# Kernel optimization log

Hardware: AMD Instinct MI355X
Metric: run time of the kernel (lower is better)

Reference implementation:

```python
import jax, jax.numpy as jnp
import numpy as np

N_NODES = 50000
N_EDGES = 1_600_000
N_REL = 8
D_IN = 128
D_OUT = 128


def _unique_edges(rng, n_nodes, n_rel, n_edges):
    # Torch module clamps the dense adjacency to 0/1, so duplicate
    # (rel, src, dst) triples collapse; generate unique edges so the
    # edge-list formulation matches exactly.
    m = 2 * n_edges
    src = rng.integers(0, n_nodes, m)
    dst = rng.integers(0, n_nodes, m)
    et = rng.integers(0, n_rel, m)
    key = (et.astype(np.int64) * n_nodes + src) * n_nodes + dst
    _, idx = np.unique(key, return_index=True)
    idx = np.sort(idx)[:n_edges]
    return src[idx], dst[idx], et[idx]


def setup_inputs() -> dict:
    key = jax.random.key(0)
    kx, kw, kr, kb = jax.random.split(key, 4)
    rng = np.random.default_rng(0)
    src, dst, et = _unique_edges(rng, N_NODES, N_REL, N_EDGES)
    bound = 1.0 / np.sqrt(D_OUT)
    return {
        "x": jax.random.normal(kx, (N_NODES, D_IN), dtype=jnp.float32),
        "edge_index": jnp.asarray(np.stack([src, dst]), dtype=jnp.int64),
        "edge_type": jnp.asarray(et, dtype=jnp.int64),
        "weight": jax.random.uniform(kw, (N_REL, D_OUT, D_IN), minval=-bound, maxval=bound, dtype=jnp.float32),
        "root": jax.random.uniform(kr, (D_OUT, D_IN), minval=-bound, maxval=bound, dtype=jnp.float32),
        "bias": jax.random.uniform(kb, (D_OUT,), minval=-bound, maxval=bound, dtype=jnp.float32),
    }


def reference(x, edge_index, edge_type, weight, root, bias):
    # Math identical to: adj[l, src, dst] = 1; adj row-normalized (mean);
    # out = sum_r norm_adj_r @ x @ W_r^T + x @ root^T + bias.
    n_rel, d_out, d_in = weight.shape
    n_nodes = x.shape[0]
    src = edge_index[0]
    dst = edge_index[1]
    seg = (edge_type * n_nodes + src).astype(jnp.int32)  # segment per (rel, node)
    num_seg = n_rel * n_nodes
    # sum of neighbor features per (relation, node): [R*N, d_in]
    agg = jax.ops.segment_sum(x[dst], seg, num_segments=num_seg)
    deg = jax.ops.segment_sum(jnp.ones((src.shape[0],), dtype=x.dtype), seg, num_segments=num_seg)
    norm = jnp.where(deg > 0, 1.0 / deg, 0.0)[:, None]  # mean aggr, nan_to_num(0)
    agg = (agg * norm).reshape(n_rel, n_nodes, d_in)
    out = jnp.einsum('rnd,rod->no', agg, weight)
    out = out + x @ root.T + bias[None]
    return out
```

## Files before the change

kernel.cpp:

```cpp
#include <hip/hip_runtime.h>


#define D 128
#define SCAN_CHUNK 2048
#define SEG_BITS 9
#define SEGS_PER_BUCKET 512
#define NBLK 256
#define NDEG 32

typedef __attribute__((ext_vector_type(8))) short short8;
typedef __attribute__((ext_vector_type(4))) float v4f;
typedef __attribute__((ext_vector_type(2))) float f32x2;
typedef __attribute__((ext_vector_type(4))) unsigned uint4v;

#define GLOAD_LDS16(gptr, lptr) \
    __builtin_amdgcn_global_load_lds((const __attribute__((address_space(1))) void*)(gptr), \
                                     (__attribute__((address_space(3))) void*)(lptr), 16, 0, 0)

__device__ __forceinline__ unsigned short f2b(float f) {
    union { float f; unsigned u; } v; v.f = f;
    unsigned r = v.u + 0x7fffu + ((v.u >> 16) & 1u);
    return (unsigned short)(r >> 16);
}
__device__ __forceinline__ float blo(unsigned u) {
    union { unsigned u; float f; } v; v.u = u << 16; return v.f;
}
__device__ __forceinline__ float bhi(unsigned u) {
    union { unsigned u; float f; } v; v.u = u & 0xffff0000u; return v.f;
}

__global__ void cvt_bf16_all(const float* __restrict__ x, long long nx,
                             const float* __restrict__ w, long long nw,
                             const float* __restrict__ root, long long nr,
                             unsigned short* __restrict__ Abuf,
                             unsigned short* __restrict__ wB, size_t SLs) {
    long long i = ((long long)blockIdx.x * blockDim.x + threadIdx.x) * 4;
    if (i < nx) {
        float4 v = *(const float4*)(x + i);
        uint2 p;
        p.x = (unsigned)f2b(v.x) | ((unsigned)f2b(v.y) << 16);
        p.y = (unsigned)f2b(v.z) | ((unsigned)f2b(v.w) << 16);
        long long n = i >> 7;
        int d = (int)(i & 127);
        size_t o = (size_t)((d >> 5) * 9 + 8) * SLs + (size_t)n * 32 + (d & 31);
        *(uint2*)(Abuf + o) = p;
        return;
    }
    const float* src;
    unsigned short* dst;
    long long j;
    if (i < nx + nw) { src = w; dst = wB; j = i - nx; }
    else if (i < nx + nw + nr) { src = root; dst = wB + nw; j = i - nx - nw; }
    else return;
    float4 v = *(const float4*)(src + j);
    uint2 p;
    p.x = (unsigned)f2b(v.x) | ((unsigned)f2b(v.y) << 16);
    p.y = (unsigned)f2b(v.z) | ((unsigned)f2b(v.w) << 16);
    *(uint2*)(dst + j) = p;
}

__global__ __launch_bounds__(256)
void histA(const int* __restrict__ ei, const int* __restrict__ et,
           int* __restrict__ blockHist, int nE, int nN, int B, int epb) {
    __shared__ int lh[1024];
    const int tid = threadIdx.x;
    for (int b = tid; b < B; b += 256) lh[b] = 0;
    __syncthreads();
    const int base = blockIdx.x * epb;
    const int lim = min(base + epb, nE);
    for (int e = base + tid * 4; e < lim; e += 1024) {
        if (e + 4 <= lim) {
            int4 s = *(const int4*)(ei + e);
            int4 t = *(const int4*)(et + e);
            atomicAdd(&lh[(t.x * nN + s.x) >> SEG_BITS], 1);
            atomicAdd(&lh[(t.y * nN + s.y) >> SEG_BITS], 1);
            atomicAdd(&lh[(t.z * nN + s.z) >> SEG_BITS], 1);
            atomicAdd(&lh[(t.w * nN + s.w) >> SEG_BITS], 1);
        } else {
            for (int k = e; k < lim; k++)
                atomicAdd(&lh[(et[k] * nN + ei[k]) >> SEG_BITS], 1);
        }
    }
    __syncthreads();
    for (int b = tid; b < B; b += 256)
        blockHist[b * NBLK + blockIdx.x] = lh[b];
}

__global__ __launch_bounds__(256)
void scan1(const int* __restrict__ in, int* __restrict__ excl,
           int* __restrict__ blockSums, int n) {
    __shared__ int t[256];
    const int tid = threadIdx.x;
    const int base = blockIdx.x * SCAN_CHUNK + tid * 8;
    int v[8];
    int tot = 0;
#pragma unroll
    for (int i = 0; i < 8; i++) {
        v[i] = (base + i < n) ? in[base + i] : 0;
        tot += v[i];
    }
    t[tid] = tot;
    __syncthreads();
    for (int off = 1; off < 256; off <<= 1) {
        int add = (tid >= off) ? t[tid - off] : 0;
        __syncthreads();
        t[tid] += add;
        __syncthreads();
    }
    int run = t[tid] - tot;
#pragma unroll
    for (int i = 0; i < 8; i++) {
        if (base + i < n) excl[base + i] = run;
        run += v[i];
    }
    if (tid == 255) blockSums[blockIdx.x] = t[255];
}

__global__ __launch_bounds__(256)
void scan2(int* __restrict__ blockSums, int nb) {
    __shared__ int t[256];
    const int tid = threadIdx.x;
    int v = (tid < nb) ? blockSums[tid] : 0;
    t[tid] = v;
    __syncthreads();
    for (int off = 1; off < 256; off <<= 1) {
        int add = (tid >= off) ? t[tid - off] : 0;
        __syncthreads();
        t[tid] += add;
        __syncthreads();
    }
    if (tid < nb) blockSums[tid] = t[tid] - v;
}

__global__ __launch_bounds__(256)
void scatterA(const int* __restrict__ ei, const int* __restrict__ et,
              const int* __restrict__ scanned, const int* __restrict__ blockSums,
              unsigned* __restrict__ bucketEdges,
              int nE, int nN, int B, int epb) {
    __shared__ int cur[1024];
    const int tid = threadIdx.x;
    for (int b = tid; b < B; b += 256) {
        int idx = b * NBLK + blockIdx.x;
        cur[b] = scanned[idx] + blockSums[idx >> 11];
    }
    __syncthreads();
    const int base = blockIdx.x * epb;
    const int lim = min(base + epb, nE);
    for (int e = base + tid * 4; e < lim; e += 1024) {
        if (e + 4 <= lim) {
            int4 s = *(const int4*)(ei + e);
            int4 t = *(const int4*)(et + e);
            int4 d = *(const int4*)(ei + nE + e);
            int sg;
            sg = t.x * nN + s.x;
            bucketEdges[atomicAdd(&cur[sg >> SEG_BITS], 1)] =
                ((unsigned)(sg & (SEGS_PER_BUCKET - 1)) << 16) | (unsigned)d.x;
            sg = t.y * nN + s.y;
            bucketEdges[atomicAdd(&cur[sg >> SEG_BITS], 1)] =
                ((unsigned)(sg & (SEGS_PER_BUCKET - 1)) << 16) | (unsigned)d.y;
            sg = t.z * nN + s.z;
            bucketEdges[atomicAdd(&cur[sg >> SEG_BITS], 1)] =
                ((unsigned)(sg & (SEGS_PER_BUCKET - 1)) << 16) | (unsigned)d.z;
            sg = t.w * nN + s.w;
            bucketEdges[atomicAdd(&cur[sg >> SEG_BITS], 1)] =
                ((unsigned)(sg & (SEGS_PER_BUCKET - 1)) << 16) | (unsigned)d.w;
        } else {
            for (int k = e; k < lim; k++) {
                int sg = et[k] * nN + ei[k];
                bucketEdges[atomicAdd(&cur[sg >> SEG_BITS], 1)] =
                    ((unsigned)(sg & (SEGS_PER_BUCKET - 1)) << 16) | (unsigned)ei[nE + k];
            }
        }
    }
}

__global__ __launch_bounds__(256)
void segOff(const unsigned* __restrict__ bucketEdges, const int* __restrict__ scanned,
            const int* __restrict__ blockSums,
            int4* __restrict__ permRec, unsigned short* __restrict__ sortedDst,
            int* __restrict__ permMax, int nE, int numSeg, int B) {
    __shared__ int lh[SEGS_PER_BUCKET];
    __shared__ int sc[256];
    __shared__ int lcur[SEGS_PER_BUCKET];
    __shared__ int dcnt[256];
    __shared__ int dbase[256];
    __shared__ int smax[32];
    const int tid = threadIdx.x;
    const int b = blockIdx.x;
    const int i0 = b * NBLK;
    const int eBase = scanned[i0] + blockSums[i0 >> 11];
    int eEnd = nE;
    if (b + 1 < B) {
        const int i1 = (b + 1) * NBLK;
        eEnd = scanned[i1] + blockSums[i1 >> 11];
    }
    const int segBase = b * SEGS_PER_BUCKET;
    const int segLim = min(SEGS_PER_BUCKET, numSeg - segBase);

    lh[2 * tid] = 0; lh[2 * tid + 1] = 0;
    dcnt[tid] = 0;
    if (tid < 32) smax[tid] = 0;
    __syncthreads();
    for (int i = eBase + tid; i < eEnd; i += 256)
        atomicAdd(&lh[bucketEdges[i] >> 16], 1);
    __syncthreads();
    const int li0 = 2 * tid, li1 = 2 * tid + 1;
    const int sub = li0 >> 6;
    int a0 = lh[li0], a1 = lh[li1];
    int b0 = min(a0, NDEG - 1), b1 = min(a1, NDEG - 1), r0 = 0, r1 = 0;
    if (li0 < segLim) r0 = atomicAdd(&dcnt[sub * NDEG + b0], 1);
    if (li1 < segLim) r1 = atomicAdd(&dcnt[sub * NDEG + b1], 1);
    sc[tid] = a0 + a1;
    __syncthreads();
    for (int o = 1; o < 256; o <<= 1) {
        int add = (tid >= o) ? sc[tid - o] : 0;
        __syncthreads();
        sc[tid] += add;
        __syncthreads();
    }
    int pairBase = sc[tid] - (a0 + a1);
    int g0 = eBase + pairBase;
    int g1 = g0 + a0;
    lcur[li0] = g0;
    lcur[li1] = g1;
    if (tid < 8) {
        int run = 0;
#pragma unroll
        for (int k = 0; k < NDEG; k++) { dbase[tid * NDEG + k] = run; run += dcnt[tid * NDEG + k]; }
    }
    __syncthreads();
    if (li0 < segLim) {
        int rk = dbase[sub * NDEG + b0] + r0;
        permRec[segBase + sub * 64 + rk] = make_int4(g0, a0, segBase + li0, 0);
        atomicMax(&smax[(sub << 2) + (rk >> 4)], a0);
    }
    if (li1 < segLim) {
        int rk = dbase[sub * NDEG + b1] + r1;
        permRec[segBase + sub * 64 + rk] = make_int4(g1, a1, segBase + li1, 0);
        atomicMax(&smax[(sub << 2) + (rk >> 4)], a1);
    }
    for (int i = eBase + tid; i < eEnd; i += 256) {
        unsigned u = bucketEdges[i];
        int pos = atomicAdd(&lcur[u >> 16], 1);
        sortedDst[pos] = (unsigned short)(u & 0xFFFFu);
    }
    __syncthreads();
    if (tid < 32) permMax[b * 32 + tid] = smax[tid];
}

__global__ __launch_bounds__(256)
void rgcn_gather(const unsigned short* __restrict__ Abase,
                 const unsigned short* __restrict__ sortedDst,
                 const int4* __restrict__ permRec,
                 const int* __restrict__ permMax,
                 unsigned short* __restrict__ Abuf, int nN, int numSeg,
                 size_t SLs, unsigned long long M) {
    const int tid = threadIdx.x;
    const int lane = tid & 63;
    const int idx4 = lane & 3;
    const int grp = lane >> 2;
    const int wv = tid >> 6;
    const int gsi0 = blockIdx.x * 128 + wv * 32 + grp;
    const int gsi1 = gsi0 + 16;
    const int sl = blockIdx.y;
    const bool v0 = (gsi0 < numSeg);
    const bool v1 = (gsi1 < numSeg);

    int4 rc0 = v0 ? permRec[gsi0] : make_int4(0, 0, 0, 0);
    int4 rc1 = v1 ? permRec[gsi1] : make_int4(0, 0, 0, 0);
    int mx0 = v0 ? permMax[gsi0 >> 4] : 0;
    int mx1 = v1 ? permMax[gsi1 >> 4] : 0;
    mx0 = __builtin_amdgcn_readfirstlane(mx0);
    mx1 = __builtin_amdgcn_readfirstlane(mx1);

    const int start0 = rc0.x, cnt0 = v0 ? rc0.y : 0, seg0 = rc0.z;
    const int start1 = rc1.x, cnt1 = v1 ? rc1.y : 0, seg1 = rc1.z;

    f32x2 a0[4], a1[4];
#pragma unroll
    for (int i = 0; i < 4; i++) { a0[i] = (f32x2){0.f, 0.f}; a1[i] = (f32x2){0.f, 0.f}; }

    const unsigned short* xSlab = Abase + (size_t)(sl * 9 + 8) * SLs + idx4 * 8;

    const int mxm = max(mx0, mx1);
    for (int b = 0; b < mxm; b += 4) {
        uint4v w0[4], w1[4];
        int myD0 = 0, myD1 = 0;
        if (b < mx0) myD0 = (b + idx4 < cnt0) ? (int)sortedDst[start0 + b + idx4] : 0;
        if (b < mx1) myD1 = (b + idx4 < cnt1) ? (int)sortedDst[start1 + b + idx4] : 0;
        if (b < mx0) {
#pragma unroll
            for (int j = 0; j < 4; j++) {
                int dst = __shfl(myD0, grp * 4 + j);
                bool act = (b + j < cnt0);
                w0[j] = act ? *(const uint4v*)(xSlab + ((size_t)dst << 5))
                            : (uint4v){0u, 0u, 0u, 0u};
            }
        }
        if (b < mx1) {
#pragma unroll
            for (int j = 0; j < 4; j++) {
                int dst = __shfl(myD1, grp * 4 + j);
                bool act = (b + j < cnt1);
                w1[j] = act ? *(const uint4v*)(xSlab + ((size_t)dst << 5))
                            : (uint4v){0u, 0u, 0u, 0u};
            }
        }
        if (b < mx0) {
#pragma unroll
            for (int j = 0; j < 4; j++) {
                f32x2 t0 = (f32x2){blo(w0[j].x), bhi(w0[j].x)};
                f32x2 t1 = (f32x2){blo(w0[j].y), bhi(w0[j].y)};
                f32x2 t2 = (f32x2){blo(w0[j].z), bhi(w0[j].z)};
                f32x2 t3 = (f32x2){blo(w0[j].w), bhi(w0[j].w)};
                asm("v_pk_add_f32 %0, %0, %1" : "+v"(a0[0]) : "v"(t0));
                asm("v_pk_add_f32 %0, %0, %1" : "+v"(a0[1]) : "v"(t1));
                asm("v_pk_add_f32 %0, %0, %1" : "+v"(a0[2]) : "v"(t2));
                asm("v_pk_add_f32 %0, %0, %1" : "+v"(a0[3]) : "v"(t3));
            }
        }
        if (b < mx1) {
#pragma unroll
            for (int j = 0; j < 4; j++) {
                f32x2 t0 = (f32x2){blo(w1[j].x), bhi(w1[j].x)};
                f32x2 t1 = (f32x2){blo(w1[j].y), bhi(w1[j].y)};
                f32x2 t2 = (f32x2){blo(w1[j].z), bhi(w1[j].z)};
                f32x2 t3 = (f32x2){blo(w1[j].w), bhi(w1[j].w)};
                asm("v_pk_add_f32 %0, %0, %1" : "+v"(a1[0]) : "v"(t0));
                asm("v_pk_add_f32 %0, %0, %1" : "+v"(a1[1]) : "v"(t1));
                asm("v_pk_add_f32 %0, %0, %1" : "+v"(a1[2]) : "v"(t2));
                asm("v_pk_add_f32 %0, %0, %1" : "+v"(a1[3]) : "v"(t3));
            }
        }
    }

    if (v0) {
        float s = cnt0 > 0 ? 1.0f / (float)cnt0 : 0.f;
        const int r = (int)(((unsigned long long)seg0 * M) >> 48);
        const int n = seg0 - r * nN;
        unsigned p0, p1, p2, p3;
        float e0, e1;
        e0 = a0[0].x * s; e1 = a0[0].y * s;
        asm("v_cvt_pk_bf16_f32 %0, %1, %2" : "=v"(p0) : "v"(e0), "v"(e1));
        e0 = a0[1].x * s; e1 = a0[1].y * s;
        asm("v_cvt_pk_bf16_f32 %0, %1, %2" : "=v"(p1) : "v"(e0), "v"(e1));
        e0 = a0[2].x * s; e1 = a0[2].y * s;
        asm("v_cvt_pk_bf16_f32 %0, %1, %2" : "=v"(p2) : "v"(e0), "v"(e1));
        e0 = a0[3].x * s; e1 = a0[3].y * s;
        asm("v_cvt_pk_bf16_f32 %0, %1, %2" : "=v"(p3) : "v"(e0), "v"(e1));
        uint4v pkt = (uint4v){p0, p1, p2, p3};
        __builtin_nontemporal_store(pkt,
            (uint4v*)(Abuf + (size_t)(sl * 9 + r) * SLs + (size_t)n * 32 + idx4 * 8));
    }
    if (v1) {
        float s = cnt1 > 0 ? 1.0f / (float)cnt1 : 0.f;
        const int r = (int)(((unsigned long long)seg1 * M) >> 48);
        const int n = seg1 - r * nN;
        unsigned p0, p1, p2, p3;
        float e0, e1;
        e0 = a1[0].x * s; e1 = a1[0].y * s;
        asm("v_cvt_pk_bf16_f32 %0, %1, %2" : "=v"(p0) : "v"(e0), "v"(e1));
        e0 = a1[1].x * s; e1 = a1[1].y * s;
        asm("v_cvt_pk_bf16_f32 %0, %1, %2" : "=v"(p1) : "v"(e0), "v"(e1));
        e0 = a1[2].x * s; e1 = a1[2].y * s;
        asm("v_cvt_pk_bf16_f32 %0, %1, %2" : "=v"(p2) : "v"(e0), "v"(e1));
        e0 = a1[3].x * s; e1 = a1[3].y * s;
        asm("v_cvt_pk_bf16_f32 %0, %1, %2" : "=v"(p3) : "v"(e0), "v"(e1));
        uint4v pkt = (uint4v){p0, p1, p2, p3};
        __builtin_nontemporal_store(pkt,
            (uint4v*)(Abuf + (size_t)(sl * 9 + r) * SLs + (size_t)n * 32 + idx4 * 8));
    }
}

__global__ __launch_bounds__(256)
void rgcn_gemm_mfma(const unsigned short* __restrict__ A,
                    const unsigned short* __restrict__ wB,
                    const float* __restrict__ bias,
                    float* __restrict__ out, int nN, int nRel, size_t SLs) {
    __shared__ __align__(16) unsigned short As[2][128 * 64];
    __shared__ __align__(16) unsigned short Bs[2][128 * 64];
    const int tid = threadIdx.x;
    const int wave = tid >> 6;
    const int lane = tid & 63;
    const int wm = wave & 1;
    const int wn = wave >> 1;
    const int m16 = lane & 15;
    const int q = lane >> 4;
    const int row0 = blockIdx.x * 128;

    v4f acc[4][4];
#pragma unroll
    for (int i = 0; i < 4; i++)
#pragma unroll
        for (int j = 0; j < 4; j++) acc[i][j] = (v4f){0.f, 0.f, 0.f, 0.f};

    const int sw = m16 & 7;
    int aoff[4][2], boff[4][2];
#pragma unroll
    for (int mt = 0; mt < 4; mt++) {
        int row = wm * 64 + mt * 16 + m16;
#pragma unroll
        for (int kb = 0; kb < 2; kb++)
            aoff[mt][kb] = row * 64 + (((kb * 4 + q) ^ sw) * 8);
    }
#pragma unroll
    for (int nt = 0; nt < 4; nt++) {
        int o = wn * 64 + nt * 16 + m16;
#pragma unroll
        for (int kb = 0; kb < 2; kb++)
            boff[nt][kb] = o * 64 + (((kb * 4 + q) ^ sw) * 8);
    }

    const int l8 = lane >> 3;
    const int gd = (lane & 7) ^ l8;
    size_t aB[4];
#pragma unroll
    for (int i = 0; i < 4; i++)
        aB[i] = (size_t)((gd >> 2) * 9) * SLs
              + (size_t)(row0 + wave * 32 + i * 8 + l8) * 32 + (gd & 3) * 8;
    const size_t bBase = (size_t)(wave * 32 + l8) * D + gd * 8;

    const int nT = 2 * (nRel + 1);

#define STAGE(buf, t) do { \
        const int s_ = (t) >> 1, h_ = (t) & 1; \
        const size_t hs_ = (size_t)h_ * 18 * SLs + (size_t)s_ * SLs; \
        const unsigned short* gb_ = wB + (size_t)s_ * (D * D) + h_ * 64 + bBase; \
        GLOAD_LDS16(A + aB[0] + hs_, &As[buf][(wave * 4 + 0) * 512]); \
        GLOAD_LDS16(A + aB[1] + hs_, &As[buf][(wave * 4 + 1) * 512]); \
        GLOAD_LDS16(A + aB[2] + hs_, &As[buf][(wave * 4 + 2) * 512]); \
        GLOAD_LDS16(A + aB[3] + hs_, &As[buf][(wave * 4 + 3) * 512]); \
        GLOAD_LDS16(gb_,        &Bs[buf][(wave * 4 + 0) * 512]); \
        GLOAD_LDS16(gb_ + 1024, &Bs[buf][(wave * 4 + 1) * 512]); \
        GLOAD_LDS16(gb_ + 2048, &Bs[buf][(wave * 4 + 2) * 512]); \
        GLOAD_LDS16(gb_ + 3072, &Bs[buf][(wave * 4 + 3) * 512]); \
    } while (0)

    STAGE(0, 0);
    __syncthreads();
    int cur = 0;
    for (int t = 0; t < nT; ++t) {
        if (t + 1 < nT) STAGE(cur ^ 1, t + 1);
        const unsigned short* Ab = As[cur];
        const unsigned short* Bb = Bs[cur];
#pragma unroll
        for (int kb = 0; kb < 2; kb++) {
            short8 a[4], b[4];
#pragma unroll
            for (int mt = 0; mt < 4; mt++)
                a[mt] = *(const short8*)&Ab[aoff[mt][kb]];
#pragma unroll
            for (int nt = 0; nt < 4; nt++)
                b[nt] = *(const short8*)&Bb[boff[nt][kb]];
#pragma unroll
            for (int mt = 0; mt < 4; mt++)
#pragma unroll
                for (int nt = 0; nt < 4; nt++)
                    acc[mt][nt] = __builtin_amdgcn_mfma_f32_16x16x32_bf16(
                        a[mt], b[nt], acc[mt][nt], 0, 0, 0);
        }
        __syncthreads();
        cur ^= 1;
    }
#undef STAGE

#pragma unroll
    for (int mt = 0; mt < 4; mt++) {
#pragma unroll
        for (int nt = 0; nt < 4; nt++) {
            int col = wn * 64 + nt * 16 + m16;
            float bi = bias[col];
#pragma unroll
            for (int reg = 0; reg < 4; reg++) {
                int rrow = row0 + wm * 64 + mt * 16 + q * 4 + reg;
                if (rrow < nN)
                    out[(size_t)rrow * D + col] = acc[mt][nt][reg] + bi;
            }
        }
    }
}

extern "C" void kernel_launch(void* const* d_in, const int* in_sizes, int n_in,
                              void* d_out, int out_size, void* d_ws, size_t ws_size,
                              hipStream_t stream) {
    const float* x    = (const float*)d_in[0];
    const int*   ei   = (const int*)d_in[1];
    const int*   et   = (const int*)d_in[2];
    const float* w    = (const float*)d_in[3];
    const float* root = (const float*)d_in[4];
    const float* bias = (const float*)d_in[5];
    float* out = (float*)d_out;

    const int nN   = in_sizes[0] / D;
    const int nE   = in_sizes[2];
    const int nRel = in_sizes[3] / (D * D);
    const int numSeg = nRel * nN;
    const int B = (numSeg + SEGS_PER_BUCKET - 1) >> SEG_BITS;
    const int nBH = B * NBLK;
    const int epb = (((nE + NBLK - 1) / NBLK) + 3) & ~3;
    const int nNalloc = (nN + 127) & ~127;
    const size_t SLs = (size_t)nNalloc * 32;
    const unsigned long long M = ((1ULL << 48) + nN - 1) / nN;

    char* p = (char*)d_ws;
    unsigned* bucketEdges   = (unsigned*)p;        p += (size_t)nE * sizeof(unsigned);
    unsigned short* sortedDst = (unsigned short*)p; p += (size_t)nE * sizeof(unsigned short);
    p = (char*)(((uintptr_t)p + 255) & ~(uintptr_t)255);
    int* blockHist = (int*)p;  p += (size_t)nBH * sizeof(int);
    int* scanned   = (int*)p;  p += (size_t)nBH * sizeof(int);
    int* blockSums = (int*)p;  p += 256 * sizeof(int);
    p = (char*)(((uintptr_t)p + 255) & ~(uintptr_t)255);
    int4* permRec  = (int4*)p; p += (size_t)numSeg * sizeof(int4);
    int* permMax   = (int*)p;  p += (size_t)B * 32 * sizeof(int);
    p = (char*)(((uintptr_t)p + 255) & ~(uintptr_t)255);
    unsigned short* wBc  = (unsigned short*)p;  p += (size_t)(nRel + 1) * D * D * sizeof(unsigned short);
    p = (char*)(((uintptr_t)p + 255) & ~(uintptr_t)255);
    unsigned short* Abuf = (unsigned short*)p;

    const int nScanBlocks = (nBH + SCAN_CHUNK - 1) / SCAN_CHUNK;

    histA<<<NBLK, 256, 0, stream>>>(ei, et, blockHist, nE, nN, B, epb);
    scan1<<<nScanBlocks, 256, 0, stream>>>(blockHist, scanned, blockSums, nBH);
    scan2<<<1, 256, 0, stream>>>(blockSums, nScanBlocks);
    scatterA<<<NBLK, 256, 0, stream>>>(ei, et, scanned, blockSums, bucketEdges, nE, nN, B, epb);
    segOff<<<B, 256, 0, stream>>>(bucketEdges, scanned, blockSums, permRec, sortedDst, permMax,
                                  nE, numSeg, B);

    long long nx = (long long)nN * D;
    long long nw = (long long)nRel * D * D;
    long long nr = (long long)D * D;
    long long ncvt = (nx + nw + nr) / 4;
    cvt_bf16_all<<<(int)((ncvt + 255) / 256), 256, 0, stream>>>(x, nx, w, nw, root, nr,
                                                                Abuf, wBc, SLs);

    dim3 gg((numSeg + 127) / 128, 4);
    rgcn_gather<<<gg, 256, 0, stream>>>(Abuf, sortedDst, permRec, permMax, Abuf, nN, numSeg,
                                        SLs, M);

    rgcn_gemm_mfma<<<(nN + 127) / 128, 256, 0, stream>>>(Abuf, wBc, bias, out, nN, nRel, SLs);
}
```

Measured before the change: 225.7 us.

## Fuse bf16 conversion into histogram launch and fold block-sum scan into consumers

The bf16 conversion of x and the weights now runs as extra blocks of the histogram kernel, so both share one launch and overlap. The one-block scan2 kernel is removed; scatterA and segOff each redo the small block-sum prefix scan in shared memory. The gather's nontemporal stores become regular stores, so Abuf may stay in cache for the GEMM. This cuts two launches and their serialization, at the cost of redundant scan work in every block and a 128-entry limit on scan blocks.

```diff
diff --git a/kernel.cpp b/kernel.cpp
--- a/kernel.cpp
+++ b/kernel.cpp
@@ -29,41 +29,42 @@
     union { unsigned u; float f; } v; v.u = u & 0xffff0000u; return v.f;
 }
 
-__global__ void cvt_bf16_all(const float* __restrict__ x, long long nx,
-                             const float* __restrict__ w, long long nw,
-                             const float* __restrict__ root, long long nr,
-                             unsigned short* __restrict__ Abuf,
-                             unsigned short* __restrict__ wB, size_t SLs) {
-    long long i = ((long long)blockIdx.x * blockDim.x + threadIdx.x) * 4;
-    if (i < nx) {
-        float4 v = *(const float4*)(x + i);
+__global__ __launch_bounds__(256)
+void histA_cvt(const int* __restrict__ ei, const int* __restrict__ et,
+               int* __restrict__ blockHist, int nE, int nN, int B, int epb,
+               const float* __restrict__ x, long long nx,
+               const float* __restrict__ w, long long nw,
+               const float* __restrict__ root, long long nr,
+               unsigned short* __restrict__ Abuf,
+               unsigned short* __restrict__ wB, size_t SLs) {
+    __shared__ int lh[1024];
+    const int tid = threadIdx.x;
+    if (blockIdx.x >= NBLK) {
+        long long i = ((long long)(blockIdx.x - NBLK) * blockDim.x + tid) * 4;
+        if (i < nx) {
+            float4 v = *(const float4*)(x + i);
+            uint2 p;
+            p.x = (unsigned)f2b(v.x) | ((unsigned)f2b(v.y) << 16);
+            p.y = (unsigned)f2b(v.z) | ((unsigned)f2b(v.w) << 16);
+            long long n = i >> 7;
+            int d = (int)(i & 127);
+            size_t o = (size_t)((d >> 5) * 9 + 8) * SLs + (size_t)n * 32 + (d & 31);
+            *(uint2*)(Abuf + o) = p;
+            return;
+        }
+        const float* src;
+        unsigned short* dst;
+        long long j;
+        if (i < nx + nw) { src = w; dst = wB; j = i - nx; }
+        else if (i < nx + nw + nr) { src = root; dst = wB + nw; j = i - nx - nw; }
+        else return;
+        float4 v = *(const float4*)(src + j);
         uint2 p;
         p.x = (unsigned)f2b(v.x) | ((unsigned)f2b(v.y) << 16);
         p.y = (unsigned)f2b(v.z) | ((unsigned)f2b(v.w) << 16);
-        long long n = i >> 7;
-        int d = (int)(i & 127);
-        size_t o = (size_t)((d >> 5) * 9 + 8) * SLs + (size_t)n * 32 + (d & 31);
-        *(uint2*)(Abuf + o) = p;
+        *(uint2*)(dst + j) = p;
         return;
     }
-    const float* src;
-    unsigned short* dst;
-    long long j;
-    if (i < nx + nw) { src = w; dst = wB; j = i - nx; }
-    else if (i < nx + nw + nr) { src = root; dst = wB + nw; j = i - nx - nw; }
-    else return;
-    float4 v = *(const float4*)(src + j);
-    uint2 p;
-    p.x = (unsigned)f2b(v.x) | ((unsigned)f2b(v.y) << 16);
-    p.y = (unsigned)f2b(v.z) | ((unsigned)f2b(v.w) << 16);
-    *(uint2*)(dst + j) = p;
-}
-
-__global__ __launch_bounds__(256)
-void histA(const int* __restrict__ ei, const int* __restrict__ et,
-           int* __restrict__ blockHist, int nE, int nN, int B, int epb) {
-    __shared__ int lh[1024];
-    const int tid = threadIdx.x;
     for (int b = tid; b < B; b += 256) lh[b] = 0;
     __syncthreads();
     const int base = blockIdx.x * epb;
@@ -117,31 +118,27 @@
 }
 
 __global__ __launch_bounds__(256)
-void scan2(int* __restrict__ blockSums, int nb) {
-    __shared__ int t[256];
-    const int tid = threadIdx.x;
-    int v = (tid < nb) ? blockSums[tid] : 0;
-    t[tid] = v;
-    __syncthreads();
-    for (int off = 1; off < 256; off <<= 1) {
-        int add = (tid >= off) ? t[tid - off] : 0;
-        __syncthreads();
-        t[tid] += add;
-        __syncthreads();
-    }
-    if (tid < nb) blockSums[tid] = t[tid] - v;
-}
-
-__global__ __launch_bounds__(256)
 void scatterA(const int* __restrict__ ei, const int* __restrict__ et,
               const int* __restrict__ scanned, const int* __restrict__ blockSums,
               unsigned* __restrict__ bucketEdges,
-              int nE, int nN, int B, int epb) {
+              int nE, int nN, int B, int epb, int nSB) {
     __shared__ int cur[1024];
+    __shared__ int bs[128];
     const int tid = threadIdx.x;
+    int myv = 0;
+    if (tid < 128) { myv = (tid < nSB) ? blockSums[tid] : 0; bs[tid] = myv; }
+    __syncthreads();
+    for (int o = 1; o < 128; o <<= 1) {
+        int add = (tid >= o && tid < 128) ? bs[tid - o] : 0;
+        __syncthreads();
+        if (tid < 128) bs[tid] += add;
+        __syncthreads();
+    }
+    if (tid < 128) bs[tid] -= myv;
+    __syncthreads();
     for (int b = tid; b < B; b += 256) {
         int idx = b * NBLK + blockIdx.x;
-        cur[b] = scanned[idx] + blockSums[idx >> 11];
+        cur[b] = scanned[idx] + bs[idx >> 11];
     }
     __syncthreads();
     const int base = blockIdx.x * epb;
@@ -178,29 +175,40 @@
 void segOff(const unsigned* __restrict__ bucketEdges, const int* __restrict__ scanned,
             const int* __restrict__ blockSums,
             int4* __restrict__ permRec, unsigned short* __restrict__ sortedDst,
-            int* __restrict__ permMax, int nE, int numSeg, int B) {
+            int* __restrict__ permMax, int nE, int numSeg, int B, int nSB) {
     __shared__ int lh[SEGS_PER_BUCKET];
     __shared__ int sc[256];
     __shared__ int lcur[SEGS_PER_BUCKET];
     __shared__ int dcnt[256];
     __shared__ int dbase[256];
     __shared__ int smax[32];
+    __shared__ int bs[128];
     const int tid = threadIdx.x;
     const int b = blockIdx.x;
+    int myv = 0;
+    if (tid < 128) { myv = (tid < nSB) ? blockSums[tid] : 0; bs[tid] = myv; }
+    lh[2 * tid] = 0; lh[2 * tid + 1] = 0;
+    dcnt[tid] = 0;
+    if (tid < 32) smax[tid] = 0;
+    __syncthreads();
+    for (int o = 1; o < 128; o <<= 1) {
+        int add = (tid >= o && tid < 128) ? bs[tid - o] : 0;
+        __syncthreads();
+        if (tid < 128) bs[tid] += add;
+        __syncthreads();
+    }
+    if (tid < 128) bs[tid] -= myv;
+    __syncthreads();
     const int i0 = b * NBLK;
-    const int eBase = scanned[i0] + blockSums[i0 >> 11];
+    const int eBase = scanned[i0] + bs[i0 >> 11];
     int eEnd = nE;
     if (b + 1 < B) {
         const int i1 = (b + 1) * NBLK;
-        eEnd = scanned[i1] + blockSums[i1 >> 11];
+        eEnd = scanned[i1] + bs[i1 >> 11];
     }
     const int segBase = b * SEGS_PER_BUCKET;
     const int segLim = min(SEGS_PER_BUCKET, numSeg - segBase);
 
-    lh[2 * tid] = 0; lh[2 * tid + 1] = 0;
-    dcnt[tid] = 0;
-    if (tid < 32) smax[tid] = 0;
-    __syncthreads();
     for (int i = eBase + tid; i < eEnd; i += 256)
         atomicAdd(&lh[bucketEdges[i] >> 16], 1);
     __syncthreads();
@@ -349,8 +357,7 @@
         e0 = a0[3].x * s; e1 = a0[3].y * s;
         asm("v_cvt_pk_bf16_f32 %0, %1, %2" : "=v"(p3) : "v"(e0), "v"(e1));
         uint4v pkt = (uint4v){p0, p1, p2, p3};
-        __builtin_nontemporal_store(pkt,
-            (uint4v*)(Abuf + (size_t)(sl * 9 + r) * SLs + (size_t)n * 32 + idx4 * 8));
+        *(uint4v*)(Abuf + (size_t)(sl * 9 + r) * SLs + (size_t)n * 32 + idx4 * 8) = pkt;
     }
     if (v1) {
         float s = cnt1 > 0 ? 1.0f / (float)cnt1 : 0.f;
@@ -367,8 +374,7 @@
         e0 = a1[3].x * s; e1 = a1[3].y * s;
         asm("v_cvt_pk_bf16_f32 %0, %1, %2" : "=v"(p3) : "v"(e0), "v"(e1));
         uint4v pkt = (uint4v){p0, p1, p2, p3};
-        __builtin_nontemporal_store(pkt,
-            (uint4v*)(Abuf + (size_t)(sl * 9 + r) * SLs + (size_t)n * 32 + idx4 * 8));
+        *(uint4v*)(Abuf + (size_t)(sl * 9 + r) * SLs + (size_t)n * 32 + idx4 * 8) = pkt;
     }
 }
 
@@ -519,19 +525,19 @@
 
     const int nScanBlocks = (nBH + SCAN_CHUNK - 1) / SCAN_CHUNK;
 
-    histA<<<NBLK, 256, 0, stream>>>(ei, et, blockHist, nE, nN, B, epb);
-    scan1<<<nScanBlocks, 256, 0, stream>>>(blockHist, scanned, blockSums, nBH);
-    scan2<<<1, 256, 0, stream>>>(blockSums, nScanBlocks);
-    scatterA<<<NBLK, 256, 0, stream>>>(ei, et, scanned, blockSums, bucketEdges, nE, nN, B, epb);
-    segOff<<<B, 256, 0, stream>>>(bucketEdges, scanned, blockSums, permRec, sortedDst, permMax,
-                                  nE, numSeg, B);
-
     long long nx = (long long)nN * D;
     long long nw = (long long)nRel * D * D;
     long long nr = (long long)D * D;
     long long ncvt = (nx + nw + nr) / 4;
-    cvt_bf16_all<<<(int)((ncvt + 255) / 256), 256, 0, stream>>>(x, nx, w, nw, root, nr,
-                                                                Abuf, wBc, SLs);
+    const int nCvtBlk = (int)((ncvt + 255) / 256);
+
+    histA_cvt<<<NBLK + nCvtBlk, 256, 0, stream>>>(ei, et, blockHist, nE, nN, B, epb,
+                                                  x, nx, w, nw, root, nr, Abuf, wBc, SLs);
+    scan1<<<nScanBlocks, 256, 0, stream>>>(blockHist, scanned, blockSums, nBH);
+    scatterA<<<NBLK, 256, 0, stream>>>(ei, et, scanned, blockSums, bucketEdges,
+                                       nE, nN, B, epb, nScanBlocks);
+    segOff<<<B, 256, 0, stream>>>(bucketEdges, scanned, blockSums, permRec, sortedDst, permMax,
+                                  nE, numSeg, B, nScanBlocks);
 
     dim3 gg((numSeg + 127) / 128, 4);
     rgcn_gather<<<gg, 256, 0, stream>>>(Abuf, sortedDst, permRec, permMax, Abuf, nN, numSeg,
```

New measurement: 229.0 us. About the same (+1.5%).
